# Performance work log

Measured on AMD Instinct MI355X. Metric: run time of the kernel, lower is better.

## Reference

```python
import jax, jax.numpy as jnp
import numpy as np

N, F_IN, H, C, E = 50000, 512, 128, 64, 800000


def setup_inputs() -> dict:
    key = jax.random.key(0)
    ks = jax.random.split(key, 20)
    stdv = 1.0 / np.sqrt(H)
    std_att = 1.0
    std_att_vec = 1.0 / np.sqrt(3.0)
    u = lambda k, shape, s: jax.random.uniform(k, shape, jnp.float32, -s, s)
    inp = {
        "x": jax.random.normal(ks[0], (N, F_IN), jnp.float32),
        "edge_row": jax.random.randint(ks[1], (E,), 0, N, jnp.int32),
        "edge_col": jax.random.randint(ks[2], (E,), 0, N, jnp.int32),
        "edge_val": jax.random.uniform(ks[3], (E,), jnp.float32) * (1.0 / 16.0),
        "weight_low": u(ks[4], (F_IN, H), stdv),
        "weight_high": u(ks[5], (F_IN, H), stdv),
        "weight_mlp": u(ks[6], (F_IN, H), stdv),
        "att_vec_low": u(ks[7], (H, 1), std_att),
        "att_vec_high": u(ks[8], (H, 1), std_att),
        "att_vec_mlp": u(ks[9], (H, 1), std_att),
        "att_vec": u(ks[10], (3, 3), std_att_vec),
        "weight_low2": u(ks[11], (H, C), stdv),
        "weight_high2": u(ks[12], (H, C), stdv),
        "weight_mlp2": u(ks[13], (H, C), stdv),
        "att_vec_low2": u(ks[14], (C, 1), std_att),
        "att_vec_high2": u(ks[15], (C, 1), std_att),
        "att_vec_mlp2": u(ks[16], (C, 1), std_att),
        "att_vec2": u(ks[17], (3, 3), std_att_vec),
    }
    return inp


def _spmm_low(row, col, val, X):
    # adj_low @ X via gather + segment-sum over edges
    return jax.ops.segment_sum(val[:, None] * X[col], row, num_segments=N)


def _attention(o_low, o_high, o_mlp, a_low, a_high, a_mlp, a_vec):
    T = 3.0
    feats = jnp.concatenate([o_low @ a_low, o_high @ a_high, o_mlp @ a_mlp], axis=1)  # [N,3]
    att = jax.nn.softmax(jax.nn.sigmoid(feats) @ a_vec / T, axis=1)
    return att[:, 0:1], att[:, 1:2], att[:, 2:3]


def _layer(X, row, col, val, W_l, W_h, W_m, a_l, a_h, a_m, a_vec):
    xl = X @ W_l
    xh = X @ W_h
    o_low = jax.nn.relu(_spmm_low(row, col, val, xl))
    o_high = jax.nn.relu(xh - _spmm_low(row, col, val, xh))  # (I - adj_low) @ xh
    o_mlp = jax.nn.relu(X @ W_m)
    al, ah, am = _attention(o_low, o_high, o_mlp, a_l, a_h, a_m, a_vec)
    return 3.0 * (al * o_low + ah * o_high + am * o_mlp)


def reference(x, edge_row, edge_col, edge_val, weight_low, weight_high, weight_mlp,
              att_vec_low, att_vec_high, att_vec_mlp, att_vec,
              weight_low2, weight_high2, weight_mlp2,
              att_vec_low2, att_vec_high2, att_vec_mlp2, att_vec2):
    h = _layer(x, edge_row, edge_col, edge_val, weight_low, weight_high, weight_mlp,
               att_vec_low, att_vec_high, att_vec_mlp, att_vec)
    out = _layer(h, edge_row, edge_col, edge_val, weight_low2, weight_high2, weight_mlp2,
                 att_vec_low2, att_vec_high2, att_vec_mlp2, att_vec2)
    return jax.nn.log_softmax(out, axis=1)
```

## Files before the change

### kernel.cpp

```cpp
#include <hip/hip_runtime.h>
#include <hip/hip_bf16.h>

#define NN 50000
#define F_IN 512
#define HH 128
#define CC 64

typedef __attribute__((ext_vector_type(8))) short short8v;
typedef __attribute__((ext_vector_type(4))) float f32x4;
typedef __attribute__((ext_vector_type(2))) float f32x2;

__device__ __forceinline__ short f2b(float f) {
    unsigned u = __builtin_bit_cast(unsigned, f);
    unsigned r = (u + 0x7fffu + ((u >> 16) & 1u)) >> 16;
    return (short)r;
}
__device__ __forceinline__ float b2f(short s) {
    unsigned u = ((unsigned)(unsigned short)s) << 16;
    return __builtin_bit_cast(float, u);
}
__device__ __forceinline__ float b2f_lo(unsigned p) {
    return __builtin_bit_cast(float, p << 16);
}
__device__ __forceinline__ float b2f_hi(unsigned p) {
    return __builtin_bit_cast(float, p & 0xffff0000u);
}

__device__ __forceinline__ f32x2 q2_lo(unsigned p) {
    return __builtin_amdgcn_cvt_pk_f32_fp8(p, false);
}
__device__ __forceinline__ f32x2 q2_hi(unsigned p) {
    return __builtin_amdgcn_cvt_pk_f32_fp8(p, true);
}

__device__ __forceinline__ int xcd_swz(int bid, int nwg) {
    int q = nwg >> 3, r = nwg & 7;
    int xcd = bid & 7, off = bid >> 3;
    return (xcd < r ? xcd * (q + 1) : r * (q + 1) + (xcd - r) * q) + off;
}

__device__ __forceinline__ void load_lds16(const short* g, short* l) {
    __builtin_amdgcn_global_load_lds(
        (const __attribute__((address_space(1))) unsigned int*)g,
        (__attribute__((address_space(3))) unsigned int*)l,
        16, 0, 0);
}

template <int K, int OUTW>
__device__ __forceinline__ void wprep_body(const float* __restrict__ W0,
                                           const float* __restrict__ W1,
                                           const float* __restrict__ W2,
                                           short* __restrict__ Bt, int id) {
    const int nth = 3 * OUTW * (K / 8);
    if (id >= nth) return;
    const int n = id / (K / 8);
    const int kq = id % (K / 8);
    constexpr int HB = OUTW / 2;
    const int t = n / OUTW;
    const int r = n % OUTW;
    int sel, c;
    if (t < 2) { sel = (r >= HB) ? 1 : 0; c = t * HB + (r % HB); }
    else       { sel = 2; c = r; }
    const float* W = sel == 0 ? W0 : (sel == 1 ? W1 : W2);
    short v[8];
#pragma unroll
    for (int j = 0; j < 8; ++j) v[j] = f2b(W[(size_t)(kq * 8 + j) * OUTW + c]);
#pragma unroll
    for (int j = 0; j < 8; ++j) Bt[(size_t)n * K + kq * 8 + j] = v[j];
}

__global__ __launch_bounds__(256) void prep0(int* __restrict__ counts, int n,
                                             const float* __restrict__ Wl,
                                             const float* __restrict__ Wh,
                                             const float* __restrict__ Wm,
                                             short* __restrict__ Bt1,
                                             const float* __restrict__ Wl2,
                                             const float* __restrict__ Wh2,
                                             const float* __restrict__ Wm2,
                                             short* __restrict__ Bt2,
                                             int nZero, int nW1) {
    const int b = blockIdx.x;
    if (b < nZero) {
        int i = b * 256 + threadIdx.x;
        if (i < n) counts[i] = 0;
    } else if (b < nZero + nW1) {
        wprep_body<F_IN, HH>(Wl, Wh, Wm, Bt1, (b - nZero) * 256 + threadIdx.x);
    } else {
        wprep_body<HH, CC>(Wl2, Wh2, Wm2, Bt2, (b - nZero - nW1) * 256 + threadIdx.x);
    }
}

__global__ __launch_bounds__(256) void hist_xconv(const int* __restrict__ erow,
                                                  int* __restrict__ counts, int E,
                                                  const float* __restrict__ x,
                                                  short* __restrict__ xb, int n8,
                                                  int nHist) {
    const int b = blockIdx.x;
    const int total = gridDim.x;
    const long hb4 = ((long)b * nHist) / total;
    const long ha4 = ((long)(b + 1) * nHist) / total;
    if (ha4 != hb4) {
        int i = (int)hb4 * 256 + threadIdx.x;
        if (i < E) atomicAdd(&counts[erow[i]], 1);
        return;
    }
    int i = (b - (int)hb4) * 256 + threadIdx.x;
    if (i >= n8) return;
    const float4* xp = (const float4*)x;
    const float4 a = xp[2 * i];
    const float4 bb = xp[2 * i + 1];
    short8v o;
    o[0] = f2b(a.x); o[1] = f2b(a.y); o[2] = f2b(a.z); o[3] = f2b(a.w);
    o[4] = f2b(bb.x); o[5] = f2b(bb.y); o[6] = f2b(bb.z); o[7] = f2b(bb.w);
    *reinterpret_cast<short8v*>(&xb[(size_t)i * 8]) = o;
}

template <int K, int BNout>
__device__ __forceinline__ void gemm_body(const short* __restrict__ A,
                                          const short* __restrict__ Bt,
                                          unsigned* __restrict__ xq,
                                          short* __restrict__ xh,
                                          short* __restrict__ xm,
                                          int M, int wg, short* smem) {
    constexpr int BM = 128, BK = 32;
    constexpr int FM = (BNout == 128) ? 4 : 2;
    constexpr int FN = 4;
    constexpr int WM = FM * 16;
    constexpr int NKT = K / BK;
    constexpr int AW = (BM * BK / 512) / 4;
    constexpr int BW_ = (BNout * BK / 512) / 4;
    constexpr int VMC = AW + BW_;
    constexpr int HALF = BM * BK + BNout * BK;
    constexpr int HB = BNout / 2;

    const int tid = threadIdx.x;
    const int lane = tid & 63;
    const int wid = tid >> 6;
    const int bm = wg / 3;
    const int bn = wg % 3;
    const int m0 = bm * BM;
    const int n0 = bn * BNout;
    const int wm = (BNout == 128) ? (wid >> 1) : wid;
    const int wn = (BNout == 128) ? (wid & 1) : 0;

    const int rl = lane >> 2;
    const int sl = (lane & 3) ^ ((lane >> 3) & 3);

    f32x4 acc[FM][FN];
#pragma unroll
    for (int i = 0; i < FM; ++i)
#pragma unroll
        for (int j = 0; j < FN; ++j) acc[i][j] = (f32x4){0.f, 0.f, 0.f, 0.f};

    auto issue = [&](int kt, int b) {
        const int k0 = kt * BK;
        short* As = smem + b * HALF;
        short* Bs = As + BM * BK;
#pragma unroll
        for (int i = 0; i < AW; ++i) {
            int g = wid * AW + i;
            int r = g * 16 + rl;
            int gr = m0 + r; if (gr >= M) gr = M - 1;
            load_lds16(&A[(size_t)gr * K + k0 + sl * 8], &As[g * 512]);
        }
#pragma unroll
        for (int i = 0; i < BW_; ++i) {
            int g = wid * BW_ + i;
            int r = g * 16 + rl;
            load_lds16(&Bt[(size_t)(n0 + r) * K + k0 + sl * 8], &Bs[g * 512]);
        }
    };

    issue(0, 0);

    const int mrow = lane & 15;
    const int kg = lane >> 4;
    for (int kt = 0; kt < NKT; ++kt) {
        const int cur = kt & 1;
        if (kt + 1 < NKT) {
            issue(kt + 1, cur ^ 1);
            asm volatile("s_waitcnt vmcnt(%0)" :: "n"(VMC) : "memory");
        } else {
            asm volatile("s_waitcnt vmcnt(0)" ::: "memory");
        }
        __builtin_amdgcn_s_barrier();
        __builtin_amdgcn_sched_barrier(0);

        const short* As = smem + cur * HALF;
        const short* Bs = As + BM * BK;
        short8v af[FM], bf[FN];
#pragma unroll
        for (int f = 0; f < FM; ++f) {
            int m = wm * WM + f * 16 + mrow;
            af[f] = *reinterpret_cast<const short8v*>(
                &As[m * 32 + ((kg ^ ((m >> 1) & 3)) << 3)]);
        }
#pragma unroll
        for (int f = 0; f < FN; ++f) {
            int nr = wn * 64 + f * 16 + mrow;
            bf[f] = *reinterpret_cast<const short8v*>(
                &Bs[nr * 32 + ((kg ^ ((nr >> 1) & 3)) << 3)]);
        }
#pragma unroll
        for (int i = 0; i < FM; ++i)
#pragma unroll
            for (int j = 0; j < FN; ++j)
                acc[i][j] = __builtin_amdgcn_mfma_f32_16x16x32_bf16(
                    af[i], bf[j], acc[i][j], 0, 0, 0);

        asm volatile("s_waitcnt lgkmcnt(0)" ::: "memory");
        __builtin_amdgcn_sched_barrier(0);
        __builtin_amdgcn_s_barrier();
    }

#pragma unroll
    for (int i = 0; i < FM; ++i)
#pragma unroll
        for (int j = 0; j < FN; ++j) {
            int cc = wn * 64 + j * 16 + (lane & 15);
#pragma unroll
            for (int e = 0; e < 4; ++e) {
                int r = wm * WM + i * 16 + (lane >> 4) * 4 + e;
                smem[r * BNout + cc] = f2b(acc[i][j][e]);
            }
        }
    __syncthreads();

    if (bn == 2) {
        constexpr int CH = BM * BNout / 8;
#pragma unroll
        for (int p = 0; p < CH / 256; ++p) {
            int idx = p * 256 + tid;
            int r = idx / (BNout / 8);
            int c8 = idx % (BNout / 8);
            int grow = m0 + r;
            if (grow < M)
                *reinterpret_cast<int4*>(&xm[(size_t)grow * BNout + c8 * 8]) =
                    *reinterpret_cast<const int4*>(&smem[r * BNout + c8 * 8]);
        }
    } else {
#pragma unroll
        for (int p = 0; p < (BM * (HB / 8)) / 256; ++p) {
            int idx = p * 256 + tid;
            int r = idx / (HB / 8);
            int c8 = idx % (HB / 8);
            int grow = m0 + r;
            if (grow < M)
                *reinterpret_cast<int4*>(&xh[(size_t)grow * BNout + bn * HB + c8 * 8]) =
                    *reinterpret_cast<const int4*>(&smem[r * BNout + HB + c8 * 8]);
        }
#pragma unroll
        for (int p = 0; p < (BM * (BNout / 4)) / 256; ++p) {
            int idx = p * 256 + tid;
            int r = idx / (BNout / 4);
            int k = idx % (BNout / 4);
            int grow = m0 + r;
            if (grow < M) {
                unsigned lw = *reinterpret_cast<const unsigned*>(&smem[r * BNout + 2 * k]);
                unsigned hw = *reinterpret_cast<const unsigned*>(&smem[r * BNout + HB + 2 * k]);
                unsigned w;
                if (BNout == 128) {
                    w = __builtin_amdgcn_cvt_pk_fp8_f32(b2f_lo(lw), b2f_hi(lw), 0, false);
                    w = __builtin_amdgcn_cvt_pk_fp8_f32(b2f_lo(hw), b2f_hi(hw), w, true);
                } else {
                    w = __builtin_amdgcn_cvt_pk_fp8_f32(b2f_lo(lw), b2f_lo(hw), 0, false);
                    w = __builtin_amdgcn_cvt_pk_fp8_f32(b2f_hi(lw), b2f_hi(hw), w, true);
                }
                xq[(size_t)grow * (BNout / 2) + bn * (BNout / 4) + k] = w;
            }
        }
    }
}

template <int BNout>
struct GemmSmem {
    static constexpr int SM1 = 2 * (128 * 32 + BNout * 32);
    static constexpr int SM2 = 128 * BNout;
    static constexpr int SZ = SM1 > SM2 ? SM1 : SM2;
};

template <int K, int BNout>
__global__ __launch_bounds__(256) void gemm_scatter(const short* __restrict__ A,
                                                    const short* __restrict__ Bt,
                                                    unsigned* __restrict__ xq,
                                                    short* __restrict__ xh,
                                                    short* __restrict__ xm,
                                                    int M, int nGemm,
                                                    const int* __restrict__ row,
                                                    const int* __restrict__ col,
                                                    const float* __restrict__ val,
                                                    int* __restrict__ cursor,
                                                    unsigned* __restrict__ edges, int E,
                                                    int nScat) {
    __shared__ short smem[GemmSmem<BNout>::SZ];

    const int total = nGemm + nScat;
    const int swz = xcd_swz(blockIdx.x, total);
    const long ns_b = ((long)swz * nScat) / total;
    const long ns_a = ((long)(swz + 1) * nScat) / total;

    if (ns_a != ns_b) {
        int i = (int)ns_b * 256 + threadIdx.x;
        if (i < E) {
            int r = row[i];
            int p = atomicAdd(&cursor[r], 1);
            unsigned rec = (unsigned)col[i] |
                           ((unsigned)(unsigned short)f2b(val[i]) << 16);
            edges[p] = rec;
        }
        return;
    }
    gemm_body<K, BNout>(A, Bt, xq, xh, xm, M, swz - (int)ns_b, smem);
}

template <int K, int BNout>
__global__ __launch_bounds__(256) void gemm_mfma(const short* __restrict__ A,
                                                 const short* __restrict__ Bt,
                                                 unsigned* __restrict__ xq,
                                                 short* __restrict__ xh,
                                                 short* __restrict__ xm,
                                                 int M) {
    __shared__ short smem[GemmSmem<BNout>::SZ];
    gemm_body<K, BNout>(A, Bt, xq, xh, xm, M, xcd_swz(blockIdx.x, gridDim.x), smem);
}

__global__ __launch_bounds__(256) void block_sums_kernel(const int* __restrict__ counts,
                                                         int* __restrict__ bsums, int n) {
    __shared__ int s[256];
    int tid = threadIdx.x;
    int i = blockIdx.x * 256 + tid;
    s[tid] = (i < n) ? counts[i] : 0;
    __syncthreads();
#pragma unroll
    for (int off = 128; off > 0; off >>= 1) {
        if (tid < off) s[tid] += s[tid + off];
        __syncthreads();
    }
    if (tid == 0) bsums[blockIdx.x] = s[0];
}

__global__ __launch_bounds__(256) void scan_bsums_kernel(int* __restrict__ bsums, int nb) {
    __shared__ int s[256];
    int t = threadIdx.x;
    int v = (t < nb) ? bsums[t] : 0;
    s[t] = v;
    __syncthreads();
#pragma unroll
    for (int off = 1; off < 256; off <<= 1) {
        int u = (t >= off) ? s[t - off] : 0;
        __syncthreads();
        s[t] += u;
        __syncthreads();
    }
    if (t < nb) bsums[t] = s[t] - v;
}

__global__ __launch_bounds__(256) void scan_final_kernel(const int* __restrict__ counts,
                                                         const int* __restrict__ bsums,
                                                         int* __restrict__ rowptr,
                                                         int* __restrict__ cursor, int n) {
    __shared__ int s[256];
    int tid = threadIdx.x;
    int i = blockIdx.x * 256 + tid;
    int v = (i < n) ? counts[i] : 0;
    s[tid] = v;
    __syncthreads();
#pragma unroll
    for (int off = 1; off < 256; off <<= 1) {
        int t = (tid >= off) ? s[tid - off] : 0;
        __syncthreads();
        s[tid] += t;
        __syncthreads();
    }
    int excl = s[tid] - v + bsums[blockIdx.x];
    if (i < n) {
        rowptr[i] = excl;
        cursor[i] = excl;
        if (i == n - 1) rowptr[n] = excl + v;
    }
}

__device__ __forceinline__ float wave_sum(float v) {
#pragma unroll
    for (int off = 32; off > 0; off >>= 1) v += __shfl_xor(v, off, 64);
    return v;
}
__device__ __forceinline__ float wave_max(float v) {
#pragma unroll
    for (int off = 32; off > 0; off >>= 1) v = fmaxf(v, __shfl_xor(v, off, 64));
    return v;
}

__global__ __launch_bounds__(256) void spmm_att1(const int* __restrict__ rowptr,
                                                 const unsigned* __restrict__ edges,
                                                 const unsigned* __restrict__ xq,
                                                 const unsigned* __restrict__ xhp,
                                                 const unsigned* __restrict__ xmp,
                                                 const float* __restrict__ a_low,
                                                 const float* __restrict__ a_high,
                                                 const float* __restrict__ a_mlp,
                                                 const float* __restrict__ av,
                                                 short* __restrict__ hb,
                                                 int n) {
    const int node = blockIdx.x * 4 + (threadIdx.x >> 6);
    const int lane = threadIdx.x & 63;
    if (node >= n) return;

    const int s = __builtin_amdgcn_readfirstlane(rowptr[node]);
    const int e = __builtin_amdgcn_readfirstlane(rowptr[node + 1]);

    float l0 = 0.f, l1 = 0.f, h0 = 0.f, h1 = 0.f;
    for (int j = s; j < e; j += 8) {
        int   cq[8];
        float vq[8];
#pragma unroll
        for (int q = 0; q < 8; ++q) {
            const int jj = min(j + q, e - 1);
            const unsigned rec = __builtin_amdgcn_readfirstlane(edges[jj]);
            cq[q] = (int)(rec & 0xffffu);
            float t = b2f((short)(rec >> 16));
            vq[q] = (j + q < e) ? t : 0.f;
        }
        unsigned p[8];
#pragma unroll
        for (int q = 0; q < 8; ++q)
            p[q] = xq[(size_t)cq[q] * 64 + lane];
#pragma unroll
        for (int q = 0; q < 8; ++q) {
            const f32x2 lo = q2_lo(p[q]);
            const f32x2 hi = q2_hi(p[q]);
            l0 += vq[q] * lo.x; l1 += vq[q] * lo.y;
            h0 += vq[q] * hi.x; h1 += vq[q] * hi.y;
        }
    }

    const unsigned xhn = xhp[(size_t)node * 64 + lane];
    const unsigned xmn = xmp[(size_t)node * 64 + lane];
    float ol0 = fmaxf(l0, 0.f);
    float ol1 = fmaxf(l1, 0.f);
    float oh0 = fmaxf(b2f_lo(xhn) - h0, 0.f);
    float oh1 = fmaxf(b2f_hi(xhn) - h1, 0.f);
    float om0 = fmaxf(b2f_lo(xmn), 0.f);
    float om1 = fmaxf(b2f_hi(xmn), 0.f);

    const float2 aL = ((const float2*)a_low)[lane];
    const float2 aH = ((const float2*)a_high)[lane];
    const float2 aM = ((const float2*)a_mlp)[lane];
    float dl = wave_sum(ol0 * aL.x + ol1 * aL.y);
    float dh = wave_sum(oh0 * aH.x + oh1 * aH.y);
    float dm = wave_sum(om0 * aM.x + om1 * aM.y);

    const float g0 = 1.f / (1.f + expf(-dl));
    const float g1 = 1.f / (1.f + expf(-dh));
    const float g2 = 1.f / (1.f + expf(-dm));
    float s0 = (g0 * av[0] + g1 * av[3] + g2 * av[6]) * (1.f / 3.f);
    float s1 = (g0 * av[1] + g1 * av[4] + g2 * av[7]) * (1.f / 3.f);
    float s2 = (g0 * av[2] + g1 * av[5] + g2 * av[8]) * (1.f / 3.f);
    float mx = fmaxf(s0, fmaxf(s1, s2));
    float e0 = expf(s0 - mx), e1 = expf(s1 - mx), e2 = expf(s2 - mx);
    float inv = 1.f / (e0 + e1 + e2);
    float at0 = e0 * inv, at1 = e1 * inv, at2 = e2 * inv;

    float ho0 = 3.f * (at0 * ol0 + at1 * oh0 + at2 * om0);
    float ho1 = 3.f * (at0 * ol1 + at1 * oh1 + at2 * om1);
    unsigned pk = (unsigned)(unsigned short)f2b(ho0) |
                  ((unsigned)(unsigned short)f2b(ho1) << 16);
    ((unsigned*)hb)[(size_t)node * 64 + lane] = pk;
}

__global__ __launch_bounds__(256) void spmm_att2(const int* __restrict__ rowptr,
                                                 const unsigned* __restrict__ edges,
                                                 const unsigned short* __restrict__ xq,
                                                 const short* __restrict__ xhp,
                                                 const short* __restrict__ xmp,
                                                 const float* __restrict__ a_low,
                                                 const float* __restrict__ a_high,
                                                 const float* __restrict__ a_mlp,
                                                 const float* __restrict__ av,
                                                 float* __restrict__ out,
                                                 int n) {
    const int node = blockIdx.x * 4 + (threadIdx.x >> 6);
    const int lane = threadIdx.x & 63;
    if (node >= n) return;

    const int s = __builtin_amdgcn_readfirstlane(rowptr[node]);
    const int e = __builtin_amdgcn_readfirstlane(rowptr[node + 1]);

    float accl = 0.f, acch = 0.f;
    for (int j = s; j < e; j += 8) {
        int   cq[8];
        float vq[8];
#pragma unroll
        for (int q = 0; q < 8; ++q) {
            const int jj = min(j + q, e - 1);
            const unsigned rec = __builtin_amdgcn_readfirstlane(edges[jj]);
            cq[q] = (int)(rec & 0xffffu);
            float t = b2f((short)(rec >> 16));
            vq[q] = (j + q < e) ? t : 0.f;
        }
        unsigned short p[8];
#pragma unroll
        for (int q = 0; q < 8; ++q)
            p[q] = xq[(size_t)cq[q] * 64 + lane];
#pragma unroll
        for (int q = 0; q < 8; ++q) {
            const f32x2 d = q2_lo((unsigned)p[q]);
            accl += vq[q] * d.x;
            acch += vq[q] * d.y;
        }
    }

    float ol = fmaxf(accl, 0.f);
    float oh = fmaxf(b2f(xhp[(size_t)node * 64 + lane]) - acch, 0.f);
    float om = fmaxf(b2f(xmp[(size_t)node * 64 + lane]), 0.f);

    float dl = wave_sum(ol * a_low[lane]);
    float dh = wave_sum(oh * a_high[lane]);
    float dm = wave_sum(om * a_mlp[lane]);

    const float g0 = 1.f / (1.f + expf(-dl));
    const float g1 = 1.f / (1.f + expf(-dh));
    const float g2 = 1.f / (1.f + expf(-dm));
    float s0 = (g0 * av[0] + g1 * av[3] + g2 * av[6]) * (1.f / 3.f);
    float s1 = (g0 * av[1] + g1 * av[4] + g2 * av[7]) * (1.f / 3.f);
    float s2 = (g0 * av[2] + g1 * av[5] + g2 * av[8]) * (1.f / 3.f);
    float mx3 = fmaxf(s0, fmaxf(s1, s2));
    float e0 = expf(s0 - mx3), e1 = expf(s1 - mx3), e2 = expf(s2 - mx3);
    float inv = 1.f / (e0 + e1 + e2);
    float at0 = e0 * inv, at1 = e1 * inv, at2 = e2 * inv;

    float o = 3.f * (at0 * ol + at1 * oh + at2 * om);

    float m = wave_max(o);
    float ex = expf(o - m);
    float su = wave_sum(ex);
    out[(size_t)node * 64 + lane] = o - m - logf(su);
}

extern "C" void kernel_launch(void* const* d_in, const int* in_sizes, int n_in,
                              void* d_out, int out_size, void* d_ws, size_t ws_size,
                              hipStream_t stream) {
    const float* x    = (const float*)d_in[0];
    const int*   erow = (const int*)d_in[1];
    const int*   ecol = (const int*)d_in[2];
    const float* eval = (const float*)d_in[3];
    const float* Wl   = (const float*)d_in[4];
    const float* Wh   = (const float*)d_in[5];
    const float* Wm   = (const float*)d_in[6];
    const float* al   = (const float*)d_in[7];
    const float* ah   = (const float*)d_in[8];
    const float* am   = (const float*)d_in[9];
    const float* av   = (const float*)d_in[10];
    const float* Wl2  = (const float*)d_in[11];
    const float* Wh2  = (const float*)d_in[12];
    const float* Wm2  = (const float*)d_in[13];
    const float* al2  = (const float*)d_in[14];
    const float* ah2  = (const float*)d_in[15];
    const float* am2  = (const float*)d_in[16];
    const float* av2  = (const float*)d_in[17];
    float* out = (float*)d_out;

    const int E = in_sizes[1];
    const int N = NN;

    short* ws    = (short*)d_ws;
    short* xb    = ws;
    short* xh1   = xb + (size_t)N * 512;
    short* xm1   = xh1 + (size_t)N * 128;
    short* hb    = xm1 + (size_t)N * 128;
    unsigned* xq1 = (unsigned*)(hb + (size_t)N * 128);
    short* Bt1   = (short*)(xq1 + (size_t)N * 64);
    short* Bt2   = Bt1 + 384 * 512;
    int*   ip    = (int*)(Bt2 + 192 * 128);
    int*   counts = ip;
    int*   rowptr = ip + N;
    int*   cursor = ip + 2 * N + 1;
    int*   bsums  = ip + 3 * N + 1;
    unsigned* edges = (unsigned*)(ip + 3 * N + 1 + 256);

    unsigned* xq2 = xq1;
    short* xh2 = xh1;
    short* xm2 = xh1 + (size_t)N * 64;

    const int NB = (N + 255) / 256;
    const int EB = (E + 255) / 256;
    const int node_blocks = (N + 3) / 4;
    const int MT = (N + 127) / 128;
    const int XCB = (N * F_IN / 8 + 255) / 256;
    const int W1B = (3 * HH * (F_IN / 8) + 255) / 256;
    const int W2B = (3 * CC * (HH / 8) + 255) / 256;
    const int nGemm1 = MT * 3;

    prep0<<<NB + W1B + W2B, 256, 0, stream>>>(counts, N, Wl, Wh, Wm, Bt1,
                                              Wl2, Wh2, Wm2, Bt2, NB, W1B);
    hist_xconv<<<EB + XCB, 256, 0, stream>>>(erow, counts, E, x, xb,
                                             N * F_IN / 8, EB);
    block_sums_kernel<<<NB, 256, 0, stream>>>(counts, bsums, N);
    scan_bsums_kernel<<<1, 256, 0, stream>>>(bsums, NB);
    scan_final_kernel<<<NB, 256, 0, stream>>>(counts, bsums, rowptr, cursor, N);

    gemm_scatter<F_IN, HH><<<nGemm1 + EB, 256, 0, stream>>>(
        xb, Bt1, xq1, xh1, xm1, N, nGemm1, erow, ecol, eval, cursor, edges, E, EB);
    spmm_att1<<<node_blocks, 256, 0, stream>>>(rowptr, edges, xq1,
                                               (const unsigned*)xh1,
                                               (const unsigned*)xm1,
                                               al, ah, am, av, hb, N);

    gemm_mfma<HH, CC><<<MT * 3, 256, 0, stream>>>(hb, Bt2, xq2, xh2, xm2, N);
    spmm_att2<<<node_blocks, 256, 0, stream>>>(rowptr, edges,
                                               (const unsigned short*)xq2,
                                               xh2, xm2,
                                               al2, ah2, am2, av2, out, N);
}
```

Baseline: 197.4 us.

## Replace per-edge global atomic scatter with two-pass bucketed counting sort

The edge scatter into CSR order is split into two passes. First, edges are grouped into 1024-row buckets using shared-memory atomics plus one global atomic per bucket per block, and written to a temporary int2 buffer. A new sort_pass2 kernel then places each bucket's edges using shared-memory row cursors. This replaces one global atomic per edge, with scattered writes, by mostly local atomics, at the cost of an extra kernel launch and a round trip through the temp buffer. Row and column are packed into 16 bits each, and 49 blocks of 1024 threads give limited parallelism in pass 2.

```diff
diff --git a/kernel.cpp b/kernel.cpp
--- a/kernel.cpp
+++ b/kernel.cpp
@@ -5,6 +5,7 @@
 #define F_IN 512
 #define HH 128
 #define CC 64
+#define NBUK 49
 
 typedef __attribute__((ext_vector_type(8))) short short8v;
 typedef __attribute__((ext_vector_type(4))) float f32x4;
@@ -289,8 +290,8 @@
                                                     const int* __restrict__ row,
                                                     const int* __restrict__ col,
                                                     const float* __restrict__ val,
-                                                    int* __restrict__ cursor,
-                                                    unsigned* __restrict__ edges, int E,
+                                                    int* __restrict__ gcur,
+                                                    int2* __restrict__ tmp, int E,
                                                     int nScat) {
     __shared__ short smem[GemmSmem<BNout>::SZ];
 
@@ -300,17 +301,70 @@
     const long ns_a = ((long)(swz + 1) * nScat) / total;
 
     if (ns_a != ns_b) {
-        int i = (int)ns_b * 256 + threadIdx.x;
-        if (i < E) {
-            int r = row[i];
-            int p = atomicAdd(&cursor[r], 1);
-            unsigned rec = (unsigned)col[i] |
-                           ((unsigned)(unsigned short)f2b(val[i]) << 16);
-            edges[p] = rec;
+        int* icnt = reinterpret_cast<int*>(smem);
+        int* ibase = icnt + 64;
+        const int tid = threadIdx.x;
+        if (tid < 64) icnt[tid] = 0;
+        __syncthreads();
+
+        const int e0 = (int)ns_b * 2048;
+        int rr[8], cc[8], slot[8], bk[8];
+        float vv[8];
+#pragma unroll
+        for (int q = 0; q < 8; ++q) {
+            int i = e0 + q * 256 + tid;
+            if (i < E) {
+                rr[q] = row[i];
+                cc[q] = col[i];
+                vv[q] = val[i];
+                bk[q] = rr[q] >> 10;
+                slot[q] = atomicAdd(&icnt[bk[q]], 1);
+            } else {
+                bk[q] = -1;
+            }
+        }
+        __syncthreads();
+        if (tid < 64) {
+            int c = icnt[tid];
+            ibase[tid] = (c > 0) ? atomicAdd(&gcur[tid], c) : 0;
+        }
+        __syncthreads();
+#pragma unroll
+        for (int q = 0; q < 8; ++q) {
+            if (bk[q] >= 0) {
+                int2 rec;
+                rec.x = rr[q] | (cc[q] << 16);
+                rec.y = __builtin_bit_cast(int, vv[q]);
+                tmp[ibase[bk[q]] + slot[q]] = rec;
+            }
         }
         return;
     }
     gemm_body<K, BNout>(A, Bt, xq, xh, xm, M, swz - (int)ns_b, smem);
+}
+
+__global__ __launch_bounds__(1024) void sort_pass2(const int* __restrict__ rowptr,
+                                                   const int2* __restrict__ tmp,
+                                                   unsigned* __restrict__ edges,
+                                                   int n) {
+    __shared__ int cur[1024];
+    const int b = blockIdx.x;
+    const int row0 = b << 10;
+    const int nrows = min(1024, n - row0);
+    const int tid = threadIdx.x;
+    if (tid < nrows) cur[tid] = rowptr[row0 + tid];
+    __syncthreads();
+
+    const int start = rowptr[row0];
+    const int end = rowptr[min(row0 + 1024, n)];
+    for (int i = start + tid; i < end; i += 1024) {
+        const int2 rec = tmp[i];
+        const int rl = rec.x & 0xffff;
+        const int cc = ((unsigned)rec.x) >> 16;
+        const float v = __builtin_bit_cast(float, rec.y);
+        const int p = atomicAdd(&cur[rl & 1023], 1);
+        edges[p] = (unsigned)cc | ((unsigned)(unsigned short)f2b(v) << 16);
+    }
 }
 
 template <int K, int BNout>
@@ -358,7 +412,7 @@
 __global__ __launch_bounds__(256) void scan_final_kernel(const int* __restrict__ counts,
                                                          const int* __restrict__ bsums,
                                                          int* __restrict__ rowptr,
-                                                         int* __restrict__ cursor, int n) {
+                                                         int* __restrict__ gcur, int n) {
     __shared__ int s[256];
     int tid = threadIdx.x;
     int i = blockIdx.x * 256 + tid;
@@ -375,7 +429,7 @@
     int excl = s[tid] - v + bsums[blockIdx.x];
     if (i < n) {
         rowptr[i] = excl;
-        cursor[i] = excl;
+        if ((i & 1023) == 0) gcur[i >> 10] = excl;
         if (i == n - 1) rowptr[n] = excl + v;
     }
 }
@@ -574,9 +628,10 @@
     int*   ip    = (int*)(Bt2 + 192 * 128);
     int*   counts = ip;
     int*   rowptr = ip + N;
-    int*   cursor = ip + 2 * N + 1;
-    int*   bsums  = ip + 3 * N + 1;
-    unsigned* edges = (unsigned*)(ip + 3 * N + 1 + 256);
+    int*   gcur   = ip + 2 * N + 1;
+    int*   bsums  = ip + 2 * N + 1 + 64;
+    unsigned* edges = (unsigned*)(ip + 2 * N + 1 + 64 + 256);
+    int2*  tmp   = (int2*)(((size_t)(edges + E) + 15) & ~(size_t)15);
 
     unsigned* xq2 = xq1;
     short* xh2 = xh1;
@@ -590,6 +645,7 @@
     const int W1B = (3 * HH * (F_IN / 8) + 255) / 256;
     const int W2B = (3 * CC * (HH / 8) + 255) / 256;
     const int nGemm1 = MT * 3;
+    const int nScat = (E + 2047) / 2048;
 
     prep0<<<NB + W1B + W2B, 256, 0, stream>>>(counts, N, Wl, Wh, Wm, Bt1,
                                               Wl2, Wh2, Wm2, Bt2, NB, W1B);
@@ -597,10 +653,11 @@
                                              N * F_IN / 8, EB);
     block_sums_kernel<<<NB, 256, 0, stream>>>(counts, bsums, N);
     scan_bsums_kernel<<<1, 256, 0, stream>>>(bsums, NB);
-    scan_final_kernel<<<NB, 256, 0, stream>>>(counts, bsums, rowptr, cursor, N);
-
-    gemm_scatter<F_IN, HH><<<nGemm1 + EB, 256, 0, stream>>>(
-        xb, Bt1, xq1, xh1, xm1, N, nGemm1, erow, ecol, eval, cursor, edges, E, EB);
+    scan_final_kernel<<<NB, 256, 0, stream>>>(counts, bsums, rowptr, gcur, N);
+
+    gemm_scatter<F_IN, HH><<<nGemm1 + nScat, 256, 0, stream>>>(
+        xb, Bt1, xq1, xh1, xm1, N, nGemm1, erow, ecol, eval, gcur, tmp, E, nScat);
+    sort_pass2<<<NBUK, 1024, 0, stream>>>(rowptr, tmp, edges, N);
     spmm_att1<<<node_blocks, 256, 0, stream>>>(rowptr, edges, xq1,
                                                (const unsigned*)xh1,
                                                (const unsigned*)xm1,
```

Result: slower. 203.3 us (+3.0%).
